# Kernel optimization log

Hardware: AMD Instinct MI355X
Metric: run time of the kernel (lower is better)

Reference implementation:

```python
import jax, jax.numpy as jnp
import numpy as np

H = 1024
V = 50257
S = 4096


def gru_cell(x, h, W_ih, W_hh, b_ih, b_hh):
    # x: (1, in), h: (1, H). PyTorch gate order: r, z, n
    gi = x @ W_ih.T + b_ih  # (1, 3H)
    gh = h @ W_hh.T + b_hh
    i_r, i_z, i_n = jnp.split(gi, 3, axis=1)
    h_r, h_z, h_n = jnp.split(gh, 3, axis=1)
    r = jax.nn.sigmoid(i_r + h_r)
    z = jax.nn.sigmoid(i_z + h_z)
    n = jnp.tanh(i_n + r * h_n)
    return (1.0 - z) * n + z * h


def setup_inputs() -> dict:
    key = jax.random.key(0)
    ks = jax.random.split(key, 16)
    s = 0.02
    return {
        "word_input": jax.random.randint(ks[0], (1,), 0, V),
        "last_context": jax.random.normal(ks[1], (1, H), jnp.float32),
        "last_hidden": jax.random.normal(ks[2], (2, 1, H), jnp.float32),
        "encoder_outputs": jax.random.normal(ks[3], (S, 1, H), jnp.float32),
        "emb": jax.random.normal(ks[4], (V, H), jnp.float32) * s,
        "W_ih0": jax.random.normal(ks[5], (3 * H, 2 * H), jnp.float32) * s,
        "W_hh0": jax.random.normal(ks[6], (3 * H, H), jnp.float32) * s,
        "b_ih0": jnp.zeros((3 * H,), jnp.float32),
        "b_hh0": jnp.zeros((3 * H,), jnp.float32),
        "W_ih1": jax.random.normal(ks[7], (3 * H, H), jnp.float32) * s,
        "W_hh1": jax.random.normal(ks[8], (3 * H, H), jnp.float32) * s,
        "b_ih1": jnp.zeros((3 * H,), jnp.float32),
        "b_hh1": jnp.zeros((3 * H,), jnp.float32),
        "W_attn": jax.random.normal(ks[9], (H, H), jnp.float32) * s,
        "b_attn": jnp.zeros((H,), jnp.float32),
        "W_out": jax.random.normal(ks[10], (V, 2 * H), jnp.float32) * s,
        "b_out": jnp.zeros((V,), jnp.float32),
    }


def reference(word_input, last_context, last_hidden, encoder_outputs,
              emb, W_ih0, W_hh0, b_ih0, b_hh0, W_ih1, W_hh1, b_ih1, b_hh1,
              W_attn, b_attn, W_out, b_out):
    # embedding lookup -> (1, H); rnn input (1, 2H)
    word_embedded = emb[word_input].reshape(1, H)
    rnn_in = jnp.concatenate([word_embedded, last_context], axis=1)
    # 2-layer GRU, single timestep (dropout inactive at eval)
    h0 = gru_cell(rnn_in, last_hidden[0], W_ih0, W_hh0, b_ih0, b_hh0)
    h1 = gru_cell(h0, last_hidden[1], W_ih1, W_hh1, b_ih1, b_hh1)
    rnn_output = h1  # (1, H)
    hidden = jnp.stack([h0, h1], axis=0)  # (2, 1, H)
    # Bahdanau-style attention, batched (replaces per-timestep Python loop)
    enc = encoder_outputs[:, 0, :]  # (S, H)
    energies = (enc @ W_attn.T + b_attn) @ rnn_output[0]  # (S,)
    attn = jax.nn.softmax(energies)  # (S,)
    attn_weights = attn.reshape(1, 1, S)
    context = (attn[None, :] @ enc)  # (1, H)
    # output projection + log-softmax over vocab
    logits = jnp.concatenate([rnn_output, context], axis=1) @ W_out.T + b_out
    output = jax.nn.log_softmax(logits, axis=1)  # (1, V)
    return output, context, hidden, attn_weights
```

## Files before the change

kernel.cpp:

```cpp
#include <hip/hip_runtime.h>
#include <math.h>

constexpr int kH  = 1024;
constexpr int kV  = 50257;
constexpr int kS  = 4096;
constexpr int kH4 = kH / 4;
constexpr int kH2 = 2 * kH;

constexpr int WS_H0     = 0;
constexpr int WS_GH1    = 1024;
constexpr int WS_H1     = 4096;
constexpr int WS_V      = 5120;
constexpr int WS_CTX    = 6144;
constexpr int WS_ATTN   = 7168;
constexpr int WS_E      = 11264;
constexpr int WS_SC     = 15360;
constexpr int WS_LOGITS = 15424;

constexpr int OUT_LOGITS = 0;
constexpr int OUT_CTX    = kV;
constexpr int OUT_HID    = kV + kH;
constexpr int OUT_ATTN   = kV + kH + 2 * kH;

__device__ __forceinline__ float wred_sum(float v) {
#pragma unroll
  for (int o = 32; o > 0; o >>= 1) v += __shfl_down(v, o, 64);
  return v;
}
__device__ __forceinline__ float wred_max(float v) {
#pragma unroll
  for (int o = 32; o > 0; o >>= 1) v = fmaxf(v, __shfl_down(v, o, 64));
  return v;
}
__device__ __forceinline__ float sigmoidf_(float x) { return 1.0f / (1.0f + __expf(-x)); }
__device__ __forceinline__ float dot4(float4 a, float4 b) {
  return a.x * b.x + a.y * b.y + a.z * b.z + a.w * b.w;
}

typedef float f32x4_t __attribute__((ext_vector_type(4)));
__device__ __forceinline__ float4 ntld(const float4* p) {
  f32x4_t v = __builtin_nontemporal_load((const f32x4_t*)p);
  return make_float4(v.x, v.y, v.z, v.w);
}

__global__ void k1_gru0_gh1(const int* __restrict__ wi_p, const float* __restrict__ lc,
                            const float* __restrict__ lh, const float* __restrict__ emb,
                            const float* __restrict__ W_ih0, const float* __restrict__ W_hh0,
                            const float* __restrict__ b_ih0, const float* __restrict__ b_hh0,
                            const float* __restrict__ W_hh1, const float* __restrict__ b_hh1,
                            float* __restrict__ ws) {
  const int wave = threadIdx.x >> 6, lane = threadIdx.x & 63;
  const int b = blockIdx.x;
  if (b < 256) {
    const int j = b * 4 + wave;
    const int wi = wi_p[0];
    const float4* embr = (const float4*)(emb + (size_t)wi * kH);
    const float4* lc4  = (const float4*)lc;
    const float4* Wr = (const float4*)(W_ih0 + (size_t)j * kH2);
    const float4* Wz = (const float4*)(W_ih0 + (size_t)(j + kH) * kH2);
    const float4* Wn = (const float4*)(W_ih0 + (size_t)(j + 2 * kH) * kH2);
    float ar = 0.f, az = 0.f, an = 0.f;
#pragma unroll
    for (int i = 0; i < 8; i++) {
      const int idx = lane + i * 64;
      const float4 xv = (idx < kH4) ? embr[idx] : lc4[idx - kH4];
      ar += dot4(ntld(Wr + idx), xv);
      az += dot4(ntld(Wz + idx), xv);
      an += dot4(ntld(Wn + idx), xv);
    }
    const float4* Ur = (const float4*)(W_hh0 + (size_t)j * kH);
    const float4* Uz = (const float4*)(W_hh0 + (size_t)(j + kH) * kH);
    const float4* Un = (const float4*)(W_hh0 + (size_t)(j + 2 * kH) * kH);
    const float4* h4 = (const float4*)lh;
    float br = 0.f, bz = 0.f, bn = 0.f;
#pragma unroll
    for (int i = 0; i < 4; i++) {
      const int idx = lane + i * 64;
      const float4 hv = h4[idx];
      br += dot4(ntld(Ur + idx), hv);
      bz += dot4(ntld(Uz + idx), hv);
      bn += dot4(ntld(Un + idx), hv);
    }
    ar = wred_sum(ar); az = wred_sum(az); an = wred_sum(an);
    br = wred_sum(br); bz = wred_sum(bz); bn = wred_sum(bn);
    if (lane == 0) {
      const float ir = ar + b_ih0[j],          hr = br + b_hh0[j];
      const float iz = az + b_ih0[j + kH],     hz = bz + b_hh0[j + kH];
      const float in_ = an + b_ih0[j + 2 * kH], hn = bn + b_hh0[j + 2 * kH];
      const float r = sigmoidf_(ir + hr);
      const float z = sigmoidf_(iz + hz);
      const float n = tanhf(in_ + r * hn);
      ws[WS_H0 + j] = (1.f - z) * n + z * lh[j];
    }
  } else {
    const int row = (b - 256) * 4 + wave;
    const float4* W  = (const float4*)(W_hh1 + (size_t)row * kH);
    const float4* h4 = (const float4*)(lh + kH);
    float a = 0.f;
#pragma unroll
    for (int i = 0; i < 4; i++) {
      const int idx = lane + i * 64;
      a += dot4(ntld(W + idx), h4[idx]);
    }
    a = wred_sum(a);
    if (lane == 0) ws[WS_GH1 + row] = a + b_hh1[row];
  }
}

__global__ void k2_gru1(const float* __restrict__ lh, const float* __restrict__ W_ih1,
                        const float* __restrict__ b_ih1, float* __restrict__ ws,
                        float* __restrict__ out) {
  const int wave = threadIdx.x >> 6, lane = threadIdx.x & 63;
  const int j = blockIdx.x * 4 + wave;
  const float4* x4 = (const float4*)(ws + WS_H0);
  const float4* Wr = (const float4*)(W_ih1 + (size_t)j * kH);
  const float4* Wz = (const float4*)(W_ih1 + (size_t)(j + kH) * kH);
  const float4* Wn = (const float4*)(W_ih1 + (size_t)(j + 2 * kH) * kH);
  float ar = 0.f, az = 0.f, an = 0.f;
#pragma unroll
  for (int i = 0; i < 4; i++) {
    const int idx = lane + i * 64;
    const float4 xv = x4[idx];
    ar += dot4(ntld(Wr + idx), xv);
    az += dot4(ntld(Wz + idx), xv);
    an += dot4(ntld(Wn + idx), xv);
  }
  ar = wred_sum(ar); az = wred_sum(az); an = wred_sum(an);
  if (lane == 0) {
    const float r = sigmoidf_(ar + b_ih1[j] + ws[WS_GH1 + j]);
    const float z = sigmoidf_(az + b_ih1[j + kH] + ws[WS_GH1 + j + kH]);
    const float n = tanhf(an + b_ih1[j + 2 * kH] + r * ws[WS_GH1 + j + 2 * kH]);
    const float h1 = (1.f - z) * n + z * lh[kH + j];
    ws[WS_H1 + j] = h1;
    out[OUT_HID + kH + j] = h1;
    out[OUT_HID + j] = ws[WS_H0 + j];
  }
  if (blockIdx.x < 4) ws[WS_V + blockIdx.x * 256 + threadIdx.x] = 0.f;
}

__global__ void k3_attnv_logh1(const float* __restrict__ W_attn, const float* __restrict__ b_attn,
                               const float* __restrict__ W_out, const float* __restrict__ b_out,
                               float* __restrict__ ws) {
  __shared__ float red[4];
  const int b = blockIdx.x, t = threadIdx.x;
  const int wave = t >> 6, lane = t & 63;
  if (b >= 65) {
    const int row = (b - 65) * 4 + wave;
    if (row >= kV) return;
    const float4* W4  = (const float4*)(W_out + (size_t)row * kH2);
    const float4* h14 = (const float4*)(ws + WS_H1);
    float a = 0.f;
#pragma unroll
    for (int i = 0; i < 4; i++) {
      const int idx = lane + i * 64;
      a += dot4(ntld(W4 + idx), h14[idx]);
    }
    a = wred_sum(a);
    if (lane == 0) ws[WS_LOGITS + row] = a + b_out[row];
    return;
  }
  if (b < 64) {
    const float4* W4 = (const float4*)W_attn;
    float4 acc = make_float4(0.f, 0.f, 0.f, 0.f);
    const int j0 = b * 16;
#pragma unroll
    for (int jj = 0; jj < 16; jj++) {
      const int j = j0 + jj;
      const float s = ws[WS_H1 + j];
      const float4 w = ntld(W4 + (size_t)j * kH4 + t);
      acc.x += s * w.x; acc.y += s * w.y; acc.z += s * w.z; acc.w += s * w.w;
    }
    atomicAdd(&ws[WS_V + 4 * t + 0], acc.x);
    atomicAdd(&ws[WS_V + 4 * t + 1], acc.y);
    atomicAdd(&ws[WS_V + 4 * t + 2], acc.z);
    atomicAdd(&ws[WS_V + 4 * t + 3], acc.w);
  } else {
    float a = 0.f;
    for (int i = t; i < kH; i += 256) a += b_attn[i] * ws[WS_H1 + i];
    const float wsum = wred_sum(a);
    if (lane == 0) red[wave] = wsum;
    __syncthreads();
    if (t == 0) ws[WS_SC + 0] = red[0] + red[1] + red[2] + red[3];
  }
}

__global__ void k4_energies(const float* __restrict__ enc, float* __restrict__ ws) {
  const int wave = threadIdx.x >> 6, lane = threadIdx.x & 63;
  const int s = blockIdx.x * 4 + wave;
  const float4* e4 = (const float4*)(enc + (size_t)s * kH);
  const float4* v4 = (const float4*)(ws + WS_V);
  float a = 0.f;
#pragma unroll
  for (int i = 0; i < 4; i++) {
    const int idx = lane + i * 64;
    a += dot4(e4[idx], v4[idx]);
  }
  a = wred_sum(a);
  if (lane == 0) ws[WS_E + s] = a + ws[WS_SC + 0];
}

__global__ void k5_softmax(float* __restrict__ ws, float* __restrict__ out) {
  __shared__ float red[16];
  const int t = threadIdx.x, lane = t & 63, wave = t >> 6;
  const float4 e = ((const float4*)(ws + WS_E))[t];
  float m = fmaxf(fmaxf(e.x, e.y), fmaxf(e.z, e.w));
  float wm = wred_max(m);
  if (lane == 0) red[wave] = wm;
  __syncthreads();
  if (wave == 0) {
    float x = (lane < 16) ? red[lane] : -INFINITY;
    x = wred_max(x);
    if (lane == 0) red[0] = x;
  }
  __syncthreads();
  m = red[0];
  __syncthreads();
  float4 ex;
  ex.x = __expf(e.x - m); ex.y = __expf(e.y - m);
  ex.z = __expf(e.z - m); ex.w = __expf(e.w - m);
  float s = ex.x + ex.y + ex.z + ex.w;
  float wsum = wred_sum(s);
  if (lane == 0) red[wave] = wsum;
  __syncthreads();
  if (wave == 0) {
    float x = (lane < 16) ? red[lane] : 0.f;
    x = wred_sum(x);
    if (lane == 0) red[0] = x;
  }
  __syncthreads();
  const float inv = 1.0f / red[0];
  float4 a4 = make_float4(ex.x * inv, ex.y * inv, ex.z * inv, ex.w * inv);
  ((float4*)(ws + WS_ATTN))[t] = a4;
  out[OUT_ATTN + 4 * t + 0] = a4.x;
  out[OUT_ATTN + 4 * t + 1] = a4.y;
  out[OUT_ATTN + 4 * t + 2] = a4.z;
  out[OUT_ATTN + 4 * t + 3] = a4.w;
  ws[WS_CTX + t] = 0.f;
}

__global__ void k6_context(const float* __restrict__ enc, float* __restrict__ ws) {
  const int b = blockIdx.x, t = threadIdx.x;
  const float4* e4 = (const float4*)enc;
  float4 acc = make_float4(0.f, 0.f, 0.f, 0.f);
  const int s0 = b * 64;
  for (int ss = 0; ss < 64; ss++) {
    const int s = s0 + ss;
    const float a = ws[WS_ATTN + s];
    const float4 ev = e4[(size_t)s * kH4 + t];
    acc.x += a * ev.x; acc.y += a * ev.y; acc.z += a * ev.z; acc.w += a * ev.w;
  }
  atomicAdd(&ws[WS_CTX + 4 * t + 0], acc.x);
  atomicAdd(&ws[WS_CTX + 4 * t + 1], acc.y);
  atomicAdd(&ws[WS_CTX + 4 * t + 2], acc.z);
  atomicAdd(&ws[WS_CTX + 4 * t + 3], acc.w);
}

__global__ void k7_logits_ctx(const float* __restrict__ W_out, float* __restrict__ ws) {
  const int wave = threadIdx.x >> 6, lane = threadIdx.x & 63;
  const int row = blockIdx.x * 4 + wave;
  if (row >= kV) return;
  const float4* W4 = (const float4*)(W_out + (size_t)row * kH2 + kH);
  const float4* c4 = (const float4*)(ws + WS_CTX);
  float a = 0.f;
#pragma unroll
  for (int i = 0; i < 4; i++) {
    const int idx = lane + i * 64;
    a += dot4(ntld(W4 + idx), c4[idx]);
  }
  a = wred_sum(a);
  if (lane == 0) ws[WS_LOGITS + row] += a;
}

__global__ void k8m_maxlse(float* __restrict__ ws) {
  __shared__ float red[16];
  const int t = threadIdx.x, lane = t & 63, wave = t >> 6;
  float m = -INFINITY;
  for (int g = t; g < kV; g += 1024) m = fmaxf(m, ws[WS_LOGITS + g]);
  m = wred_max(m);
  if (lane == 0) red[wave] = m;
  __syncthreads();
  if (wave == 0) {
    float x = (lane < 16) ? red[lane] : -INFINITY;
    x = wred_max(x);
    if (lane == 0) red[0] = x;
  }
  __syncthreads();
  const float gm = red[0];
  __syncthreads();
  float s = 0.f;
  for (int g = t; g < kV; g += 1024) s += __expf(ws[WS_LOGITS + g] - gm);
  s = wred_sum(s);
  if (lane == 0) red[wave] = s;
  __syncthreads();
  if (t == 0) {
    float gs = 0.f;
#pragma unroll
    for (int i = 0; i < 16; i++) gs += red[i];
    ws[WS_SC + 1] = gm;
    ws[WS_SC + 2] = logf(gs);
  }
}

__global__ void k8c_output(const float* __restrict__ ws, float* __restrict__ out) {
  const int g = blockIdx.x * 256 + threadIdx.x;
  const float shift = ws[WS_SC + 1] + ws[WS_SC + 2];
  if (g < kV) out[OUT_LOGITS + g] = ws[WS_LOGITS + g] - shift;
  if (g < kH) out[OUT_CTX + g] = ws[WS_CTX + g];
}

extern "C" void kernel_launch(void* const* d_in, const int* in_sizes, int n_in,
                              void* d_out, int out_size, void* d_ws, size_t ws_size,
                              hipStream_t stream) {
  const int*   wi     = (const int*)d_in[0];
  const float* lc     = (const float*)d_in[1];
  const float* lh     = (const float*)d_in[2];
  const float* enc    = (const float*)d_in[3];
  const float* emb    = (const float*)d_in[4];
  const float* W_ih0  = (const float*)d_in[5];
  const float* W_hh0  = (const float*)d_in[6];
  const float* b_ih0  = (const float*)d_in[7];
  const float* b_hh0  = (const float*)d_in[8];
  const float* W_ih1  = (const float*)d_in[9];
  const float* W_hh1  = (const float*)d_in[10];
  const float* b_ih1  = (const float*)d_in[11];
  const float* b_hh1  = (const float*)d_in[12];
  const float* W_attn = (const float*)d_in[13];
  const float* b_attn = (const float*)d_in[14];
  const float* W_out  = (const float*)d_in[15];
  const float* b_out  = (const float*)d_in[16];
  float* out = (float*)d_out;
  float* ws  = (float*)d_ws;

  constexpr int kLogitBlocks = (kV + 3) / 4;

  k1_gru0_gh1<<<1024, 256, 0, stream>>>(wi, lc, lh, emb, W_ih0, W_hh0, b_ih0, b_hh0,
                                        W_hh1, b_hh1, ws);
  k2_gru1<<<256, 256, 0, stream>>>(lh, W_ih1, b_ih1, ws, out);
  k3_attnv_logh1<<<65 + kLogitBlocks, 256, 0, stream>>>(W_attn, b_attn, W_out, b_out, ws);
  k4_energies<<<1024, 256, 0, stream>>>(enc, ws);
  k5_softmax<<<1, 1024, 0, stream>>>(ws, out);
  k6_context<<<64, 256, 0, stream>>>(enc, ws);
  k7_logits_ctx<<<kLogitBlocks, 256, 0, stream>>>(W_out, ws);
  k8m_maxlse<<<1, 1024, 0, stream>>>(ws);
  k8c_output<<<(kV + 255) / 256, 256, 0, stream>>>(ws, out);
}
```

Baseline: 694.1 us.

## Fuse attention pipeline into one persistent kernel with grid barriers

Merges the attention-vector, energies, softmax and context kernels into a single 256-block kernel that uses atomic-counter grid barriers, keeping per-block energies in LDS. The max/log-sum-exp and output kernels are fused the same way using two barriers. The logit GEMV kernels now handle two rows per wave. This cuts kernel launches and workspace round trips. In exchange it depends on every block being co-resident for the spin barriers, and it relies on the counters being reset by an earlier kernel.

```diff
diff --git a/kernel.cpp b/kernel.cpp
--- a/kernel.cpp
+++ b/kernel.cpp
@@ -12,10 +12,13 @@
 constexpr int WS_H1     = 4096;
 constexpr int WS_V      = 5120;
 constexpr int WS_CTX    = 6144;
-constexpr int WS_ATTN   = 7168;
-constexpr int WS_E      = 11264;
-constexpr int WS_SC     = 15360;
-constexpr int WS_LOGITS = 15424;
+constexpr int WS_SC     = 7168;
+constexpr int WS_PM2    = 7184;
+constexpr int WS_GS2    = 7440;
+constexpr int WS_PM8    = 7456;
+constexpr int WS_GS8    = 7712;
+constexpr int WS_CNT    = 7728;
+constexpr int WS_LOGITS = 7744;
 
 constexpr int OUT_LOGITS = 0;
 constexpr int OUT_CTX    = kV;
@@ -41,6 +44,19 @@
 __device__ __forceinline__ float4 ntld(const float4* p) {
   f32x4_t v = __builtin_nontemporal_load((const f32x4_t*)p);
   return make_float4(v.x, v.y, v.z, v.w);
+}
+
+__device__ __forceinline__ void gsync(int* cnt, int target) {
+  __syncthreads();
+  __threadfence();
+  if (threadIdx.x == 0) {
+    atomicAdd(cnt, 1);
+    while (__hip_atomic_load(cnt, __ATOMIC_RELAXED, __HIP_MEMORY_SCOPE_AGENT) < target) {
+      __builtin_amdgcn_s_sleep(2);
+    }
+  }
+  __syncthreads();
+  __threadfence();
 }
 
 __global__ void k1_gru0_gh1(const int* __restrict__ wi_p, const float* __restrict__ lc,
@@ -84,12 +100,9 @@
     ar = wred_sum(ar); az = wred_sum(az); an = wred_sum(an);
     br = wred_sum(br); bz = wred_sum(bz); bn = wred_sum(bn);
     if (lane == 0) {
-      const float ir = ar + b_ih0[j],          hr = br + b_hh0[j];
-      const float iz = az + b_ih0[j + kH],     hz = bz + b_hh0[j + kH];
-      const float in_ = an + b_ih0[j + 2 * kH], hn = bn + b_hh0[j + 2 * kH];
-      const float r = sigmoidf_(ir + hr);
-      const float z = sigmoidf_(iz + hz);
-      const float n = tanhf(in_ + r * hn);
+      const float r = sigmoidf_(ar + b_ih0[j] + br + b_hh0[j]);
+      const float z = sigmoidf_(az + b_ih0[j + kH] + bz + b_hh0[j + kH]);
+      const float n = tanhf(an + b_ih0[j + 2 * kH] + r * (bn + b_hh0[j + 2 * kH]));
       ws[WS_H0 + j] = (1.f - z) * n + z * lh[j];
     }
   } else {
@@ -111,6 +124,7 @@
                         const float* __restrict__ b_ih1, float* __restrict__ ws,
                         float* __restrict__ out) {
   const int wave = threadIdx.x >> 6, lane = threadIdx.x & 63;
+  const int t = threadIdx.x;
   const int j = blockIdx.x * 4 + wave;
   const float4* x4 = (const float4*)(ws + WS_H0);
   const float4* Wr = (const float4*)(W_ih1 + (size_t)j * kH);
@@ -135,36 +149,57 @@
     out[OUT_HID + kH + j] = h1;
     out[OUT_HID + j] = ws[WS_H0 + j];
   }
-  if (blockIdx.x < 4) ws[WS_V + blockIdx.x * 256 + threadIdx.x] = 0.f;
-}
-
-__global__ void k3_attnv_logh1(const float* __restrict__ W_attn, const float* __restrict__ b_attn,
-                               const float* __restrict__ W_out, const float* __restrict__ b_out,
-                               float* __restrict__ ws) {
-  __shared__ float red[4];
+  if (blockIdx.x < 4) {
+    ws[WS_V + blockIdx.x * 256 + t] = 0.f;
+  } else if (blockIdx.x < 8) {
+    ws[WS_CTX + (blockIdx.x - 4) * 256 + t] = 0.f;
+  } else if (blockIdx.x == 8) {
+    if (t < 16) ws[WS_GS2 + t] = 0.f;
+    else if (t >= 32 && t < 48) ws[WS_GS8 + (t - 32)] = 0.f;
+    else if (t >= 64 && t < 66) ((int*)ws)[WS_CNT + (t - 64)] = 0;
+  }
+}
+
+__global__ void ks1_logits_h1(const float* __restrict__ W_out, const float* __restrict__ b_out,
+                              float* __restrict__ ws) {
+  const int wave = threadIdx.x >> 6, lane = threadIdx.x & 63;
+  const int r0 = blockIdx.x * 8 + wave * 2;
+  if (r0 >= kV) return;
+  const int r1 = (r0 + 1 < kV) ? r0 + 1 : r0;
+  const float4* A = (const float4*)(W_out + (size_t)r0 * kH2);
+  const float4* B = (const float4*)(W_out + (size_t)r1 * kH2);
+  const float4* x4 = (const float4*)(ws + WS_H1);
+  float a0 = 0.f, a1 = 0.f;
+#pragma unroll
+  for (int i = 0; i < 4; i++) {
+    const int idx = lane + i * 64;
+    const float4 xv = x4[idx];
+    a0 += dot4(ntld(A + idx), xv);
+    a1 += dot4(ntld(B + idx), xv);
+  }
+  a0 = wred_sum(a0); a1 = wred_sum(a1);
+  if (lane == 0) {
+    ws[WS_LOGITS + r0] = a0 + b_out[r0];
+    if (r1 != r0) ws[WS_LOGITS + r1] = a1 + b_out[r1];
+  }
+}
+
+__global__ void kattn_fused(const float* __restrict__ enc, const float* __restrict__ W_attn,
+                            const float* __restrict__ b_attn, float* __restrict__ ws,
+                            float* __restrict__ out) {
+  __shared__ float lds_e[16];
+  __shared__ float lds_u[16];
+  __shared__ float redl[4];
   const int b = blockIdx.x, t = threadIdx.x;
   const int wave = t >> 6, lane = t & 63;
-  if (b >= 65) {
-    const int row = (b - 65) * 4 + wave;
-    if (row >= kV) return;
-    const float4* W4  = (const float4*)(W_out + (size_t)row * kH2);
-    const float4* h14 = (const float4*)(ws + WS_H1);
-    float a = 0.f;
-#pragma unroll
-    for (int i = 0; i < 4; i++) {
-      const int idx = lane + i * 64;
-      a += dot4(ntld(W4 + idx), h14[idx]);
-    }
-    a = wred_sum(a);
-    if (lane == 0) ws[WS_LOGITS + row] = a + b_out[row];
-    return;
-  }
-  if (b < 64) {
+  int* cnt = ((int*)ws) + WS_CNT + 0;
+
+  {
     const float4* W4 = (const float4*)W_attn;
     float4 acc = make_float4(0.f, 0.f, 0.f, 0.f);
-    const int j0 = b * 16;
-#pragma unroll
-    for (int jj = 0; jj < 16; jj++) {
+    const int j0 = b * 4;
+#pragma unroll
+    for (int jj = 0; jj < 4; jj++) {
       const int j = j0 + jj;
       const float s = ws[WS_H1 + j];
       const float4 w = ntld(W4 + (size_t)j * kH4 + t);
@@ -174,138 +209,157 @@
     atomicAdd(&ws[WS_V + 4 * t + 1], acc.y);
     atomicAdd(&ws[WS_V + 4 * t + 2], acc.z);
     atomicAdd(&ws[WS_V + 4 * t + 3], acc.w);
-  } else {
-    float a = 0.f;
-    for (int i = t; i < kH; i += 256) a += b_attn[i] * ws[WS_H1 + i];
-    const float wsum = wred_sum(a);
-    if (lane == 0) red[wave] = wsum;
-    __syncthreads();
-    if (t == 0) ws[WS_SC + 0] = red[0] + red[1] + red[2] + red[3];
-  }
-}
-
-__global__ void k4_energies(const float* __restrict__ enc, float* __restrict__ ws) {
+    if (b == 0) {
+      float a = 0.f;
+      for (int i = t; i < kH; i += 256) a += b_attn[i] * ws[WS_H1 + i];
+      a = wred_sum(a);
+      if (lane == 0) redl[wave] = a;
+      __syncthreads();
+      if (t == 0) ws[WS_SC + 0] = redl[0] + redl[1] + redl[2] + redl[3];
+    }
+  }
+  gsync(cnt, 256);
+
+  {
+    const float4* v4 = (const float4*)(ws + WS_V);
+    const float cc = ws[WS_SC + 0];
+    const int sbase = b * 16 + wave * 4;
+#pragma unroll
+    for (int rr = 0; rr < 4; rr += 2) {
+      const int s = sbase + rr;
+      const float4* ea = (const float4*)(enc + (size_t)s * kH);
+      const float4* eb = ea + kH4;
+      float a0 = 0.f, a1 = 0.f;
+#pragma unroll
+      for (int i = 0; i < 4; i++) {
+        const int idx = lane + i * 64;
+        const float4 vv = v4[idx];
+        a0 += dot4(ea[idx], vv);
+        a1 += dot4(eb[idx], vv);
+      }
+      a0 = wred_sum(a0); a1 = wred_sum(a1);
+      if (lane == 0) {
+        lds_e[wave * 4 + rr]     = a0 + cc;
+        lds_e[wave * 4 + rr + 1] = a1 + cc;
+      }
+    }
+    __syncthreads();
+    if (t == 0) {
+      float m = lds_e[0];
+#pragma unroll
+      for (int i = 1; i < 16; i++) m = fmaxf(m, lds_e[i]);
+      ws[WS_PM2 + b] = m;
+    }
+  }
+  gsync(cnt, 512);
+
+  float gm;
+  {
+    float pm = ws[WS_PM2 + t];
+    float wm = wred_max(pm);
+    if (lane == 0) redl[wave] = wm;
+    __syncthreads();
+    gm = fmaxf(fmaxf(redl[0], redl[1]), fmaxf(redl[2], redl[3]));
+    __syncthreads();
+    if (t < 16) lds_u[t] = __expf(lds_e[t] - gm);
+    __syncthreads();
+    if (t == 0) {
+      float s16 = 0.f;
+#pragma unroll
+      for (int i = 0; i < 16; i++) s16 += lds_u[i];
+      atomicAdd(&ws[WS_GS2 + (b & 15)], s16);
+    }
+  }
+  gsync(cnt, 768);
+
+  {
+    if (t < 16) lds_e[t] = ws[WS_GS2 + t];
+    __syncthreads();
+    float tot = 0.f;
+#pragma unroll
+    for (int i = 0; i < 16; i++) tot += lds_e[i];
+    const float inv = 1.0f / tot;
+    const float4* e4 = (const float4*)enc;
+    float4 acc = make_float4(0.f, 0.f, 0.f, 0.f);
+    const int s0 = b * 16;
+#pragma unroll
+    for (int ss = 0; ss < 16; ss++) {
+      const int s = s0 + ss;
+      const float a = lds_u[ss] * inv;
+      const float4 ev = e4[(size_t)s * kH4 + t];
+      acc.x += a * ev.x; acc.y += a * ev.y; acc.z += a * ev.z; acc.w += a * ev.w;
+    }
+    atomicAdd(&ws[WS_CTX + 4 * t + 0], acc.x);
+    atomicAdd(&ws[WS_CTX + 4 * t + 1], acc.y);
+    atomicAdd(&ws[WS_CTX + 4 * t + 2], acc.z);
+    atomicAdd(&ws[WS_CTX + 4 * t + 3], acc.w);
+    if (t < 16) out[OUT_ATTN + s0 + t] = lds_u[t] * inv;
+  }
+}
+
+__global__ void ks2_logits_ctx(const float* __restrict__ W_out, float* __restrict__ ws) {
   const int wave = threadIdx.x >> 6, lane = threadIdx.x & 63;
-  const int s = blockIdx.x * 4 + wave;
-  const float4* e4 = (const float4*)(enc + (size_t)s * kH);
-  const float4* v4 = (const float4*)(ws + WS_V);
-  float a = 0.f;
+  const int r0 = blockIdx.x * 8 + wave * 2;
+  if (r0 >= kV) return;
+  const int r1 = (r0 + 1 < kV) ? r0 + 1 : r0;
+  const float4* A = (const float4*)(W_out + (size_t)r0 * kH2 + kH);
+  const float4* B = (const float4*)(W_out + (size_t)r1 * kH2 + kH);
+  const float4* c4 = (const float4*)(ws + WS_CTX);
+  float a0 = 0.f, a1 = 0.f;
 #pragma unroll
   for (int i = 0; i < 4; i++) {
     const int idx = lane + i * 64;
-    a += dot4(e4[idx], v4[idx]);
-  }
-  a = wred_sum(a);
-  if (lane == 0) ws[WS_E + s] = a + ws[WS_SC + 0];
-}
-
-__global__ void k5_softmax(float* __restrict__ ws, float* __restrict__ out) {
-  __shared__ float red[16];
-  const int t = threadIdx.x, lane = t & 63, wave = t >> 6;
-  const float4 e = ((const float4*)(ws + WS_E))[t];
-  float m = fmaxf(fmaxf(e.x, e.y), fmaxf(e.z, e.w));
-  float wm = wred_max(m);
-  if (lane == 0) red[wave] = wm;
-  __syncthreads();
-  if (wave == 0) {
-    float x = (lane < 16) ? red[lane] : -INFINITY;
-    x = wred_max(x);
-    if (lane == 0) red[0] = x;
-  }
-  __syncthreads();
-  m = red[0];
-  __syncthreads();
-  float4 ex;
-  ex.x = __expf(e.x - m); ex.y = __expf(e.y - m);
-  ex.z = __expf(e.z - m); ex.w = __expf(e.w - m);
-  float s = ex.x + ex.y + ex.z + ex.w;
-  float wsum = wred_sum(s);
-  if (lane == 0) red[wave] = wsum;
-  __syncthreads();
-  if (wave == 0) {
-    float x = (lane < 16) ? red[lane] : 0.f;
-    x = wred_sum(x);
-    if (lane == 0) red[0] = x;
-  }
-  __syncthreads();
-  const float inv = 1.0f / red[0];
-  float4 a4 = make_float4(ex.x * inv, ex.y * inv, ex.z * inv, ex.w * inv);
-  ((float4*)(ws + WS_ATTN))[t] = a4;
-  out[OUT_ATTN + 4 * t + 0] = a4.x;
-  out[OUT_ATTN + 4 * t + 1] = a4.y;
-  out[OUT_ATTN + 4 * t + 2] = a4.z;
-  out[OUT_ATTN + 4 * t + 3] = a4.w;
-  ws[WS_CTX + t] = 0.f;
-}
-
-__global__ void k6_context(const float* __restrict__ enc, float* __restrict__ ws) {
+    const float4 xv = c4[idx];
+    a0 += dot4(ntld(A + idx), xv);
+    a1 += dot4(ntld(B + idx), xv);
+  }
+  a0 = wred_sum(a0); a1 = wred_sum(a1);
+  if (lane == 0) {
+    ws[WS_LOGITS + r0] += a0;
+    if (r1 != r0) ws[WS_LOGITS + r1] += a1;
+  }
+}
+
+__global__ void k8_lse_out(float* __restrict__ ws, float* __restrict__ out) {
+  __shared__ float redl[4];
+  __shared__ float lds16[16];
   const int b = blockIdx.x, t = threadIdx.x;
-  const float4* e4 = (const float4*)enc;
-  float4 acc = make_float4(0.f, 0.f, 0.f, 0.f);
-  const int s0 = b * 64;
-  for (int ss = 0; ss < 64; ss++) {
-    const int s = s0 + ss;
-    const float a = ws[WS_ATTN + s];
-    const float4 ev = e4[(size_t)s * kH4 + t];
-    acc.x += a * ev.x; acc.y += a * ev.y; acc.z += a * ev.z; acc.w += a * ev.w;
-  }
-  atomicAdd(&ws[WS_CTX + 4 * t + 0], acc.x);
-  atomicAdd(&ws[WS_CTX + 4 * t + 1], acc.y);
-  atomicAdd(&ws[WS_CTX + 4 * t + 2], acc.z);
-  atomicAdd(&ws[WS_CTX + 4 * t + 3], acc.w);
-}
-
-__global__ void k7_logits_ctx(const float* __restrict__ W_out, float* __restrict__ ws) {
-  const int wave = threadIdx.x >> 6, lane = threadIdx.x & 63;
-  const int row = blockIdx.x * 4 + wave;
-  if (row >= kV) return;
-  const float4* W4 = (const float4*)(W_out + (size_t)row * kH2 + kH);
-  const float4* c4 = (const float4*)(ws + WS_CTX);
-  float a = 0.f;
-#pragma unroll
-  for (int i = 0; i < 4; i++) {
-    const int idx = lane + i * 64;
-    a += dot4(ntld(W4 + idx), c4[idx]);
-  }
-  a = wred_sum(a);
-  if (lane == 0) ws[WS_LOGITS + row] += a;
-}
-
-__global__ void k8m_maxlse(float* __restrict__ ws) {
-  __shared__ float red[16];
-  const int t = threadIdx.x, lane = t & 63, wave = t >> 6;
-  float m = -INFINITY;
-  for (int g = t; g < kV; g += 1024) m = fmaxf(m, ws[WS_LOGITS + g]);
-  m = wred_max(m);
-  if (lane == 0) red[wave] = m;
-  __syncthreads();
-  if (wave == 0) {
-    float x = (lane < 16) ? red[lane] : -INFINITY;
-    x = wred_max(x);
-    if (lane == 0) red[0] = x;
-  }
-  __syncthreads();
-  const float gm = red[0];
-  __syncthreads();
-  float s = 0.f;
-  for (int g = t; g < kV; g += 1024) s += __expf(ws[WS_LOGITS + g] - gm);
-  s = wred_sum(s);
-  if (lane == 0) red[wave] = s;
-  __syncthreads();
-  if (t == 0) {
-    float gs = 0.f;
-#pragma unroll
-    for (int i = 0; i < 16; i++) gs += red[i];
-    ws[WS_SC + 1] = gm;
-    ws[WS_SC + 2] = logf(gs);
-  }
-}
-
-__global__ void k8c_output(const float* __restrict__ ws, float* __restrict__ out) {
-  const int g = blockIdx.x * 256 + threadIdx.x;
-  const float shift = ws[WS_SC + 1] + ws[WS_SC + 2];
-  if (g < kV) out[OUT_LOGITS + g] = ws[WS_LOGITS + g] - shift;
-  if (g < kH) out[OUT_CTX + g] = ws[WS_CTX + g];
+  const int wave = t >> 6, lane = t & 63;
+  int* cnt = ((int*)ws) + WS_CNT + 1;
+  const int g = b * 256 + t;
+  const float x = (g < kV) ? ws[WS_LOGITS + g] : -INFINITY;
+  {
+    float m = wred_max(x);
+    if (lane == 0) redl[wave] = m;
+    __syncthreads();
+    if (t == 0) ws[WS_PM8 + b] = fmaxf(fmaxf(redl[0], redl[1]), fmaxf(redl[2], redl[3]));
+  }
+  gsync(cnt, 197);
+  float gm;
+  {
+    float pm = (t < 197) ? ws[WS_PM8 + t] : -INFINITY;
+    float wm = wred_max(pm);
+    if (lane == 0) redl[wave] = wm;
+    __syncthreads();
+    gm = fmaxf(fmaxf(redl[0], redl[1]), fmaxf(redl[2], redl[3]));
+    __syncthreads();
+    const float e = (g < kV) ? __expf(x - gm) : 0.f;
+    float s = wred_sum(e);
+    if (lane == 0) redl[wave] = s;
+    __syncthreads();
+    if (t == 0) atomicAdd(&ws[WS_GS8 + (b & 15)], redl[0] + redl[1] + redl[2] + redl[3]);
+  }
+  gsync(cnt, 394);
+  {
+    if (t < 16) lds16[t] = ws[WS_GS8 + t];
+    __syncthreads();
+    float tot = 0.f;
+#pragma unroll
+    for (int i = 0; i < 16; i++) tot += lds16[i];
+    const float shift = gm + logf(tot);
+    if (g < kV) out[OUT_LOGITS + g] = x - shift;
+    if (g < kH) out[OUT_CTX + g] = ws[WS_CTX + g];
+  }
 }
 
 extern "C" void kernel_launch(void* const* d_in, const int* in_sizes, int n_in,
@@ -331,16 +385,13 @@
   float* out = (float*)d_out;
   float* ws  = (float*)d_ws;
 
-  constexpr int kLogitBlocks = (kV + 3) / 4;
+  constexpr int kStreamBlocks = (kV + 7) / 8;
 
   k1_gru0_gh1<<<1024, 256, 0, stream>>>(wi, lc, lh, emb, W_ih0, W_hh0, b_ih0, b_hh0,
                                         W_hh1, b_hh1, ws);
   k2_gru1<<<256, 256, 0, stream>>>(lh, W_ih1, b_ih1, ws, out);
-  k3_attnv_logh1<<<65 + kLogitBlocks, 256, 0, stream>>>(W_attn, b_attn, W_out, b_out, ws);
-  k4_energies<<<1024, 256, 0, stream>>>(enc, ws);
-  k5_softmax<<<1, 1024, 0, stream>>>(ws, out);
-  k6_context<<<64, 256, 0, stream>>>(enc, ws);
-  k7_logits_ctx<<<kLogitBlocks, 256, 0, stream>>>(W_out, ws);
-  k8m_maxlse<<<1, 1024, 0, stream>>>(ws);
-  k8c_output<<<(kV + 255) / 256, 256, 0, stream>>>(ws, out);
-}
+  ks1_logits_h1<<<kStreamBlocks, 256, 0, stream>>>(W_out, b_out, ws);
+  kattn_fused<<<256, 256, 0, stream>>>(enc, W_attn, b_attn, ws, out);
+  ks2_logits_ctx<<<kStreamBlocks, 256, 0, stream>>>(W_out, ws);
+  k8_lse_out<<<197, 256, 0, stream>>>(ws, out);
+}
```

After: 886.8 us. 27.8% more time.
